# Performance work log

Hardware: AMD Instinct MI355X
Metric: run time of the kernel (lower is better)

The kernel has to match this reference:

```python
import jax, jax.numpy as jnp
import numpy as np

B, NB, V1, V2, S, J, D, F = 32, 10, 3, 3, 2, 25, 3, 8
DIN = D * F          # 24
H1, H2 = 2 * DIN, 3 * DIN  # 48, 72
NFEAT, NCLASS = 256, 60
EPS = 1e-5


def _layernorm(h, g, b):
    m = jnp.mean(h, axis=-1, keepdims=True)
    v = jnp.mean(jnp.square(h - m), axis=-1, keepdims=True)
    return (h - m) * jax.lax.rsqrt(v + EPS) * g + b


def setup_inputs() -> dict:
    key = jax.random.key(0)
    ks = jax.random.split(key, 12)
    x = jax.random.normal(ks[0], (B, NB, V1, V2, S * J, D, F), dtype=jnp.float32)
    a = jax.random.uniform(ks[1], (J, J), dtype=jnp.float32)
    adj = a / jnp.sum(a, axis=1, keepdims=True)  # row-normalized dense adjacency
    sc = 0.05
    return {
        "x": x,
        "adj": adj,
        "W1": sc * jax.random.normal(ks[2], (DIN, H1), jnp.float32),
        "b1": jnp.zeros((H1,), jnp.float32),
        "g1": jnp.ones((H1,), jnp.float32),
        "be1": jnp.zeros((H1,), jnp.float32),
        "W2": sc * jax.random.normal(ks[3], (H1, H2), jnp.float32),
        "b2": jnp.zeros((H2,), jnp.float32),
        "g2": jnp.ones((H2,), jnp.float32),
        "be2": jnp.zeros((H2,), jnp.float32),
        "W3": sc * jax.random.normal(ks[4], (H2, NFEAT), jnp.float32),
        "b3": jnp.zeros((NFEAT,), jnp.float32),
        "g3": jnp.ones((NFEAT,), jnp.float32),
        "be3": jnp.zeros((NFEAT,), jnp.float32),
        "Wc": sc * jax.random.normal(ks[5], (J * NFEAT, NCLASS), jnp.float32),
        "bc": jnp.zeros((NCLASS,), jnp.float32),
        "batch_size": B,
        "degree": 4,
        "nclass": NCLASS,
        "alpha": 0.2,
    }


def _sgc_precompute(f0, adj, degree, alpha):
    # f0: [..., J, NFEAT]; repeated sparse-style propagation with accumulation
    def step(carry, _):
        f, acc = carry
        f = jnp.einsum('ij,...jf->...if', adj, f)
        acc = acc + (1.0 - alpha) * f + alpha * f0
        return (f, acc), None
    (_, acc), _ = jax.lax.scan(step, (f0, jnp.zeros_like(f0)), None, length=degree)
    return acc / degree


def reference(x, adj, W1, b1, g1, be1, W2, b2, g2, be2, W3, b3, g3, be3,
              Wc, bc, batch_size, degree, nclass, alpha):
    # split joints into (subject, joint) and flatten (D, F) per joint -> [B,NB,V1,V2,S,J,DIN]
    h = x.reshape(B, NB, V1, V2, S, J, DIN)
    h = jax.nn.relu(_layernorm(h @ W1 + b1, g1, be1))
    h = jax.nn.relu(_layernorm(h @ W2 + b2, g2, be2))
    h = _layernorm(h @ W3 + b3, g3, be3)            # dropout is identity in eval
    h = _sgc_precompute(h, adj, degree, alpha)       # [B,NB,V1,V2,S,J,NFEAT]
    vec = h.reshape(B, NB, V1, V2, S, J * NFEAT)
    logits = vec @ Wc + bc                            # [B,NB,V1,V2,S,NCLASS]
    block_mean = jnp.mean(logits, axis=4)             # mean over subjects
    pred = jnp.mean(block_mean, axis=(1, 2, 3))       # [B, NCLASS]
    return block_mean, pred
```

## Files before the change

### kernel.cpp

```cpp
#include <hip/hip_runtime.h>
#include <hip/hip_bf16.h>

typedef __hip_bfloat16 bf16t;
typedef _Float16 half_t;
typedef __attribute__((ext_vector_type(2))) _Float16 half2v;
typedef __attribute__((ext_vector_type(8))) _Float16 half8v;
typedef __attribute__((ext_vector_type(4))) float f32x4;
typedef unsigned int uint32;

#define BB   32
#define NC   60
#define NROW 2880
#define EPSF 1e-5f
#define ALPHA 0.2f
#define DEG  4

#define WS_M_OFF    256
#define WS_PW_OFF   4096
#define WS_W3BF_OFF 28672
#define WS_W2BF_OFF 77824
#define WS_W1BF_OFF 88064
#define WS_WCP_OFF  101376
#define WS_WCPF_OFF 869376
#define WS_PART_OFF 1688576
#define WS_GH3_OFF  7586816
#define WS_NEED     44450816ULL

#define P_W1  0
#define P_B1  1152
#define P_G1  1200
#define P_BE1 1248
#define P_W2  1296
#define P_B2  4752
#define P_G2  4824
#define P_BE2 4896
#define P_B3  4968
#define P_G3  5224
#define P_BE3 5480
#define P_BC  5736
#define P_TOT 5796
#define R_W3E (P_TOT+24576)
#define R_W2E (R_W3E+5120)
#define R_W1E (R_W2E+1536)

#define LB_H3L 0
#define LB_A1  12800
#define LB_CS  12800
#define LB_A2  22016
#define LB_H3H 22016
#define LB_STW 35328
#define LB_ST2 37376
#define LDS_FTOT 9472

__device__ __forceinline__ float ldin(const void* p, int i, int isbf){
  return isbf ? __bfloat162float(((const bf16t*)p)[i]) : ((const float*)p)[i];
}
__device__ __forceinline__ void stout(void* p, int i, int isbf, float v){
  if(isbf) ((bf16t*)p)[i] = __float2bfloat16(v);
  else     ((float*)p)[i] = v;
}
__device__ __forceinline__ half2v u2h2(uint32 u){
  half2v h; __builtin_memcpy(&h,&u,4); return h;
}
__device__ __forceinline__ uint32 pk2u(float a, float b){
  auto r = __builtin_amdgcn_cvt_pkrtz(a, b);
  uint32 u; __builtin_memcpy(&u,&r,4); return u;
}

__global__ void k0_prep(const void* x, const void* adj, int* flagp, float* M){
  __shared__ float A[625], P[625], Q[625], Ss[625];
  __shared__ int cnt, flg;
  int t = threadIdx.x;
  if(t==0) cnt = 0;
  __syncthreads();
  {
    const unsigned short* xb = (const unsigned short*)x;
    unsigned short u = xb[2*t];
    int e = (u>>7)&0xFF;
    if(e>=100 && e<=141) atomicAdd(&cnt,1);
  }
  __syncthreads();
  if(t==0){ flg = (cnt>=160)?1:0; flagp[0]=flg; }
  __syncthreads();
  int isbf = flg;
  for(int i=t;i<625;i+=256){ float a=ldin(adj,i,isbf); A[i]=a; P[i]=a; Ss[i]=a; }
  __syncthreads();
  for(int d=1; d<DEG; ++d){
    for(int o=t;o<625;o+=256){
      int i=o/25, j=o%25; float acc=0.f;
      for(int k=0;k<25;k++) acc += A[i*25+k]*P[k*25+j];
      Q[o]=acc;
    }
    __syncthreads();
    for(int o=t;o<625;o+=256){ P[o]=Q[o]; Ss[o]+=Q[o]; }
    __syncthreads();
  }
  const float coef = (1.0f-ALPHA)/(float)DEG;
  for(int o=t;o<625;o+=256){
    int i=o/25, j=o%25;
    M[o] = (i==j ? ALPHA : 0.0f) + coef*Ss[o];
  }
}

__global__ void k1_all(const void* W1,const void* b1,const void* g1,const void* be1,
                       const void* W2,const void* b2,const void* g2,const void* be2,
                       const void* W3,const void* b3,const void* g3,const void* be3,
                       const void* bc, const int* flagp,
                       float* pw, half_t* W3bf, half_t* W2bf, half_t* W1bf){
  int isbf = flagp[0];
  int o = blockIdx.x*256 + threadIdx.x;
  if(o < P_TOT){
    const void* src; int loc;
    if      (o < P_B1 ) { src=W1;  loc=o;        }
    else if (o < P_G1 ) { src=b1;  loc=o-P_B1;   }
    else if (o < P_BE1) { src=g1;  loc=o-P_G1;   }
    else if (o < P_W2 ) { src=be1; loc=o-P_BE1;  }
    else if (o < P_B2 ) { src=W2;  loc=o-P_W2;   }
    else if (o < P_G2 ) { src=b2;  loc=o-P_B2;   }
    else if (o < P_BE2) { src=g2;  loc=o-P_G2;   }
    else if (o < P_B3 ) { src=be2; loc=o-P_BE2;  }
    else if (o < P_G3 ) { src=b3;  loc=o-P_B3;   }
    else if (o < P_BE3) { src=g3;  loc=o-P_G3;   }
    else if (o < P_BC ) { src=be3; loc=o-P_BE3;  }
    else                { src=bc;  loc=o-P_BC;   }
    pw[o] = ldin(src, loc, isbf);
  } else if(o < R_W3E){
    int o2 = o - P_TOT;
    int ct = o2/1536, rem = o2 - ct*1536;
    int kt = rem/512, rem2 = rem - kt*512;
    int l = rem2>>3, j = rem2&7;
    int k = kt*32 + ((l>>4)<<3) + j;
    int col = (ct<<4) + (l&15);
    float v = (k<72) ? ldin(W3, k*256+col, isbf) : 0.f;
    W3bf[o2] = (half_t)v;
  } else if(o < R_W2E){
    int o2 = o - R_W3E;
    int ct = o2/1024, rem = o2 - ct*1024;
    int kt = rem/512, rem2 = rem - kt*512;
    int l = rem2>>3, j = rem2&7;
    int k = kt*32 + ((l>>4)<<3) + j;
    int col = (ct<<4) + (l&15);
    float v = (k<48 && col<72) ? ldin(W2, k*72+col, isbf) : 0.f;
    W2bf[o2] = (half_t)v;
  } else if(o < R_W1E){
    int o2 = o - R_W2E;
    int ct = o2/512, rem2 = o2 - ct*512;
    int l = rem2>>3, j = rem2&7;
    int k = ((l>>4)<<3) + j;
    int col = (ct<<4) + (l&15);
    float v = (k<24) ? ldin(W1, k*48+col, isbf) : 0.f;
    W1bf[o2] = (half_t)v;
  }
}

__global__ void k2_fold(const void* Wc, const float* M, const int* flagp, half_t* Wcp4){
  int isbf = flagp[0];
  int o = blockIdx.x*256 + threadIdx.x;
  if(o >= 384000) return;
  int grp = o>>4, hw = o&15;
  int kt = grp/15, cg = grp - kt*15;
  int p = hw>>3, cl = (hw>>1)&3, e = hw&1;
  int fl = kt*4 + 2*p + e;
  int j = fl>>8, f = fl&255;
  int c = cg*4 + cl;
  float acc = 0.f;
  for(int i=0;i<25;i++) acc += M[i*25+j]*ldin(Wc, (i*256+f)*60 + c, isbf);
  Wcp4[o] = (half_t)(0.5f*acc);
}

__global__ void k2_foldf(const void* Wc, const float* M, const int* flagp, half_t* Wcpf){
  int isbf = flagp[0];
  int o = blockIdx.x*256 + threadIdx.x;
  int j = o&7, l = (o>>3)&63, nt = (o>>9)&3, kst = o>>11;
  int k = kst*32 + ((l>>4)<<3) + j;
  int c = nt*16 + (l&15);
  float acc = 0.f;
  if(c < 60){
    int jj = k>>8, f = k&255;
    for(int i=0;i<25;i++) acc += M[i*25+jj]*ldin(Wc, (i*256+f)*60 + c, isbf);
  }
  Wcpf[o] = (half_t)(0.5f*acc);
}

template<bool FUSED>
__global__ __launch_bounds__(256,4) void k3_t(const void* x, const float* pw,
                                              const half_t* W3bf_, const half_t* W2bf_,
                                              const half_t* W1bf_,
                                              const unsigned short* Wcp4,
                                              const int* flagp, void* out, uint32* gH3d){
  __shared__ float sm[LDS_FTOT];
  char* smb = (char*)sm;
  half_t* H3L = (half_t*)(smb + LB_H3L);
  half_t* H3H = (half_t*)(smb + LB_H3H);
  half_t* A1h = (half_t*)(smb + LB_A1);
  half_t* A2h = (half_t*)(smb + LB_A2);
  half_t* XH  = A2h;
  float*  stw = (float*)(smb + LB_STW);
  float*  st2 = (float*)(smb + LB_ST2);
  float*  cs  = (float*)(smb + LB_CS);
  uint32* A1w = (uint32*)A1h;
  const unsigned short* W3u = (const unsigned short*)W3bf_;
  const unsigned short* W2u = (const unsigned short*)W2bf_;
  const unsigned short* W1u = (const unsigned short*)W1bf_;

  int t = threadIdx.x, bid = blockIdx.x;
  int l = t&63, w = t>>6, cb = l&15, g4 = l>>4;
  int isbf = flagp[0];
  const float* b1=pw+P_B1;  const float* g1=pw+P_G1;  const float* be1=pw+P_BE1;
  const float* b2=pw+P_B2;  const float* g2=pw+P_G2;  const float* be2=pw+P_BE2;
  const float* b3=pw+P_B3;  const float* g3=pw+P_G3;  const float* be3=pw+P_BE3;
  const float* bc=pw+P_BC;

  for(int o=t;o<512;o+=256){ int r=o>>3, dc=24+(o&7); A1w[r*36+dc]=0; }
  {
    int xoff = bid*1200;
    for(int i=t;i<2560;i+=256){
      int r=i/40, c=i-(i/40)*40;
      float v = (r<50 && c<24) ? ldin(x, xoff + r*24+c, isbf) : 0.f;
      XH[i] = (half_t)v;
    }
  }
  __syncthreads();

  {
    f32x4 acc1[3];
    float g1v[3], be1v[3];
    #pragma unroll
    for(int ct=0;ct<3;ct++){
      int col = ct*16 + cb;
      float b = b1[col]; g1v[ct]=g1[col]; be1v[ct]=be1[col];
      acc1[ct][0]=b; acc1[ct][1]=b; acc1[ct][2]=b; acc1[ct][3]=b;
    }
    half8v a = *(const half8v*)(XH + (w*16 + cb)*40 + (g4<<3));
    #pragma unroll
    for(int ct=0;ct<3;ct++){
      half8v b = *(const half8v*)(W1u + (ct*64 + l)*8);
      acc1[ct] = __builtin_amdgcn_mfma_f32_16x16x32_f16(a, b, acc1[ct], 0,0,0);
    }
    __syncthreads();
    #pragma unroll
    for(int r=0;r<4;r++){
      float s1 = acc1[0][r]+acc1[1][r]+acc1[2][r];
      float s2 = acc1[0][r]*acc1[0][r]+acc1[1][r]*acc1[1][r]+acc1[2][r]*acc1[2][r];
      #pragma unroll
      for(int d=1;d<16;d<<=1){ s1+=__shfl_xor(s1,d,64); s2+=__shfl_xor(s2,d,64); }
      float m = s1*(1.f/48.f);
      float var = s2*(1.f/48.f)-m*m;
      float rs = rsqrtf(var+EPSF);
      int row = w*16 + (g4<<2) + r;
      #pragma unroll
      for(int ct=0;ct<3;ct++){
        float val = (acc1[ct][r]-m)*rs*g1v[ct]+be1v[ct];
        A1h[row*72 + ct*16 + cb] = (half_t)fmaxf(val,0.f);
      }
    }
  }
  __syncthreads();

  {
    f32x4 acc2[5];
    #pragma unroll
    for(int ct=0;ct<5;ct++){
      int col = ct*16 + cb;
      float b = (col<72) ? b2[col] : 0.f;
      acc2[ct][0]=b; acc2[ct][1]=b; acc2[ct][2]=b; acc2[ct][3]=b;
    }
    #pragma unroll
    for(int kt=0;kt<2;kt++){
      half8v a = *(const half8v*)(A1h + (w*16 + cb)*72 + kt*32 + (g4<<3));
      #pragma unroll
      for(int ct=0;ct<5;ct++){
        half8v b = *(const half8v*)(W2u + ((ct*2+kt)*64 + l)*8);
        acc2[ct] = __builtin_amdgcn_mfma_f32_16x16x32_f16(a, b, acc2[ct], 0,0,0);
      }
    }
    __syncthreads();
    int valid4 = (cb<8);
    #pragma unroll
    for(int r=0;r<4;r++){
      float s1 = acc2[0][r]+acc2[1][r]+acc2[2][r]+acc2[3][r] + (valid4?acc2[4][r]:0.f);
      float s2 = acc2[0][r]*acc2[0][r]+acc2[1][r]*acc2[1][r]
               + acc2[2][r]*acc2[2][r]+acc2[3][r]*acc2[3][r]
               + (valid4?acc2[4][r]*acc2[4][r]:0.f);
      #pragma unroll
      for(int d=1;d<16;d<<=1){ s1+=__shfl_xor(s1,d,64); s2+=__shfl_xor(s2,d,64); }
      float m = s1*(1.f/72.f);
      float var = s2*(1.f/72.f)-m*m;
      float rs = rsqrtf(var+EPSF);
      int grow = w*16 + (g4<<2) + r;
      #pragma unroll
      for(int ct=0;ct<5;ct++){
        int col = ct*16 + cb;
        if(ct<4 || valid4){
          float val = (acc2[ct][r]-m)*rs*g2[col]+be2[col];
          A2h[grow*104+col] = (half_t)fmaxf(val,0.f);
        }
      }
    }
    uint32* A2w = (uint32*)A2h;
    for(int o=l;o<192;o+=64){ int rr = w*16 + o/12, dc = 36 + (o - (o/12)*12); A2w[rr*52+dc]=0; }
  }
  __syncthreads();

  #pragma unroll 1
  for(int p=0;p<2;p++){
    f32x4 acc[2][4];
    #pragma unroll
    for(int nt=0;nt<4;nt++){
      float b3c = b3[w*64 + nt*16 + cb];
      #pragma unroll
      for(int m2=0;m2<2;m2++){ acc[m2][nt][0]=b3c; acc[m2][nt][1]=b3c; acc[m2][nt][2]=b3c; acc[m2][nt][3]=b3c; }
    }
    #pragma unroll
    for(int kt=0;kt<3;kt++){
      half8v a[2];
      #pragma unroll
      for(int m2=0;m2<2;m2++)
        a[m2] = *(const half8v*)(A2h + ((p*2+m2)*16+cb)*104 + kt*32 + (g4<<3));
      #pragma unroll
      for(int nt=0;nt<4;nt++){
        int ct = w*4 + nt;
        half8v b = *(const half8v*)(W3u + ((ct*3+kt)*64 + l)*8);
        #pragma unroll
        for(int m2=0;m2<2;m2++)
          acc[m2][nt] = __builtin_amdgcn_mfma_f32_16x16x32_f16(a[m2], b, acc[m2][nt], 0,0,0);
      }
    }
    __syncthreads();
    #pragma unroll
    for(int m2=0;m2<2;m2++){
      #pragma unroll
      for(int r=0;r<4;r++){
        int row = (p*2+m2)*16 + (g4<<2) + r;
        float s1 = acc[m2][0][r]+acc[m2][1][r]+acc[m2][2][r]+acc[m2][3][r];
        float s2 = acc[m2][0][r]*acc[m2][0][r]+acc[m2][1][r]*acc[m2][1][r]
                 + acc[m2][2][r]*acc[m2][2][r]+acc[m2][3][r]*acc[m2][3][r];
        #pragma unroll
        for(int d=1;d<16;d<<=1){ s1+=__shfl_xor(s1,d,64); s2+=__shfl_xor(s2,d,64); }
        if(cb==0){
          stw[row*8 + w*2]   = s1;
          stw[row*8 + w*2+1] = s2;
        }
        if(row<50){
          #pragma unroll
          for(int nt=0;nt<4;nt++){
            int col = w*64 + nt*16 + cb;
            if(row<25) H3L[row*256+col]      = (half_t)acc[m2][nt][r];
            else       H3H[(row-25)*256+col] = (half_t)acc[m2][nt][r];
          }
        }
      }
    }
  }
  __syncthreads();
  if(t<64){
    float S1 = stw[t*8+0]+stw[t*8+2]+stw[t*8+4]+stw[t*8+6];
    float S2 = stw[t*8+1]+stw[t*8+3]+stw[t*8+5]+stw[t*8+7];
    float m = S1*(1.f/256.f);
    float var = S2*(1.f/256.f)-m*m;
    st2[2*t]=m; st2[2*t+1]=rsqrtf(var+EPSF);
  }
  __syncthreads();
  {
    uint32* H3l32 = (uint32*)H3L;
    uint32* H3h32 = (uint32*)H3H;
    int cp = t & 127, ro = t>>7;
    float ga=g3[2*cp], gb=g3[2*cp+1], ba=be3[2*cp], bb=be3[2*cp+1];
    for(int r=ro; r<25; r+=2){
      uint32 lo = H3l32[r*128+cp], hi = H3h32[r*128+cp];
      float ml=st2[2*r], rl=st2[2*r+1];
      float mh=st2[2*(r+25)], rh=st2[2*(r+25)+1];
      half2v l2=u2h2(lo), h2=u2h2(hi);
      float v0 = ((float)l2[0]-ml)*rl*ga+ba + ((float)h2[0]-mh)*rh*ga+ba;
      float v1 = ((float)l2[1]-ml)*rl*gb+bb + ((float)h2[1]-mh)*rh*gb+bb;
      if(FUSED) H3l32[r*128+cp] = pk2u(v0, v1);
      else      gH3d[(size_t)bid*3200 + r*128 + cp] = pk2u(v0, v1);
    }
  }
  if constexpr (FUSED){
    __syncthreads();
    {
      int cgc = (cb<15)?cb:14;
      int ktbase = w*400 + g4*100;
      const unsigned short* H3u = (const unsigned short*)H3L;
      float a0=0.f,a1=0.f,a2=0.f,a3=0.f;
      for(int i=0;i<100;i++){
        int kt = ktbase + i;
        uint2 hq = *(const uint2*)(H3u + kt*4);
        const uint4* qp = (const uint4*)(Wcp4 + (size_t)(kt*15+cgc)*16);
        uint4 wa = qp[0], wb = qp[1];
        half2v h01 = u2h2(hq.x), h23 = u2h2(hq.y);
        a0 = __builtin_amdgcn_fdot2(h01, u2h2(wa.x), a0, false);
        a0 = __builtin_amdgcn_fdot2(h23, u2h2(wb.x), a0, false);
        a1 = __builtin_amdgcn_fdot2(h01, u2h2(wa.y), a1, false);
        a1 = __builtin_amdgcn_fdot2(h23, u2h2(wb.y), a1, false);
        a2 = __builtin_amdgcn_fdot2(h01, u2h2(wa.z), a2, false);
        a2 = __builtin_amdgcn_fdot2(h23, u2h2(wb.z), a2, false);
        a3 = __builtin_amdgcn_fdot2(h01, u2h2(wa.w), a3, false);
        a3 = __builtin_amdgcn_fdot2(h23, u2h2(wb.w), a3, false);
      }
      a0 += __shfl_xor(a0,16,64); a0 += __shfl_xor(a0,32,64);
      a1 += __shfl_xor(a1,16,64); a1 += __shfl_xor(a1,32,64);
      a2 += __shfl_xor(a2,16,64); a2 += __shfl_xor(a2,32,64);
      a3 += __shfl_xor(a3,16,64); a3 += __shfl_xor(a3,32,64);
      if(l<15){
        cs[w*60 + l*4 + 0] = a0;
        cs[w*60 + l*4 + 1] = a1;
        cs[w*60 + l*4 + 2] = a2;
        cs[w*60 + l*4 + 3] = a3;
      }
    }
    __syncthreads();
    if(t<NC){
      float v = cs[t]+cs[60+t]+cs[120+t]+cs[180+t] + bc[t];
      stout(out, bid*NC+t, isbf, v);
    }
  }
}

__global__ __launch_bounds__(256) void k5_gemm(const half_t* gH3, const half_t* Wcpf,
                                               float* part){
  int bx = blockIdx.x, ky = blockIdx.y;
  int t = threadIdx.x, l = t&63, w = t>>6, cb = l&15, g4 = l>>4;
  const unsigned short* H = (const unsigned short*)gH3;
  const unsigned short* W = (const unsigned short*)Wcpf;
  int base = bx*64 + w*16;
  f32x4 acc[4];
  #pragma unroll
  for(int nt=0;nt<4;nt++){ acc[nt][0]=0.f; acc[nt][1]=0.f; acc[nt][2]=0.f; acc[nt][3]=0.f; }
  int kst0 = ky*25;
  for(int ks=0;ks<25;ks++){
    int kst = kst0 + ks;
    half8v a = *(const half8v*)(H + (size_t)(base+cb)*6400 + kst*32 + (g4<<3));
    #pragma unroll
    for(int nt=0;nt<4;nt++){
      half8v b = *(const half8v*)(W + ((kst*4+nt)*64 + l)*8);
      acc[nt] = __builtin_amdgcn_mfma_f32_16x16x32_f16(a, b, acc[nt], 0,0,0);
    }
  }
  #pragma unroll
  for(int nt=0;nt<4;nt++){
    #pragma unroll
    for(int r=0;r<4;r++){
      int inst = base + (g4<<2) + r;
      part[((size_t)ky*NROW + inst)*64 + nt*16 + cb] = acc[nt][r];
    }
  }
}

__global__ void k4b_out(const float* part, const float* pw, const int* flagp, void* out){
  int o = blockIdx.x*256 + threadIdx.x;
  if(o >= NROW*NC) return;
  int inst = o/NC, c = o - inst*NC;
  float v = pw[P_BC + c];
  #pragma unroll
  for(int ky=0;ky<8;ky++) v += part[((size_t)ky*NROW + inst)*64 + c];
  stout(out, o, flagp[0], v);
}

__global__ void k4_pred(const void* bm, const int* flagp, void* out){
  int b = blockIdx.x, t = threadIdx.x;
  int isbf = flagp[0];
  if(t<NC){
    float acc=0.f;
    for(int r=0;r<90;r++) acc += ldin(bm, (b*90+r)*NC+t, isbf);
    stout(out, NROW*NC + b*NC + t, isbf, acc*(1.f/90.f));
  }
}

extern "C" void kernel_launch(void* const* d_in, const int* in_sizes, int n_in,
                              void* d_out, int out_size, void* d_ws, size_t ws_size,
                              hipStream_t stream){
  const void* x   = d_in[0];
  const void* adj = d_in[1];
  char* ws = (char*)d_ws;
  int*     flagp = (int*)ws;
  float*   M     = (float*)(ws + WS_M_OFF);
  float*   pw    = (float*)(ws + WS_PW_OFF);
  half_t*  W3bf  = (half_t*)(ws + WS_W3BF_OFF);
  half_t*  W2bf  = (half_t*)(ws + WS_W2BF_OFF);
  half_t*  W1bf  = (half_t*)(ws + WS_W1BF_OFF);
  half_t*  Wcp4  = (half_t*)(ws + WS_WCP_OFF);
  half_t*  Wcpf  = (half_t*)(ws + WS_WCPF_OFF);
  float*   part  = (float*)(ws + WS_PART_OFF);
  half_t*  gH3   = (half_t*)(ws + WS_GH3_OFF);
  bool fast = (ws_size >= WS_NEED);

  k0_prep<<<1,256,0,stream>>>(x, adj, flagp, M);
  k1_all<<<(R_W1E+255)/256,256,0,stream>>>(d_in[2],d_in[3],d_in[4],d_in[5],
                                           d_in[6],d_in[7],d_in[8],d_in[9],
                                           d_in[10],d_in[11],d_in[12],d_in[13],
                                           d_in[15], flagp, pw, W3bf, W2bf, W1bf);
  if(fast){
    k2_foldf<<<1600,256,0,stream>>>(d_in[14], M, flagp, Wcpf);
    k3_t<false><<<NROW,256,0,stream>>>(x, pw, W3bf, W2bf, W1bf,
                                       (const unsigned short*)nullptr, flagp, d_out,
                                       (uint32*)gH3);
    dim3 g5(45,8);
    k5_gemm<<<g5,256,0,stream>>>(gH3, Wcpf, part);
    k4b_out<<<(NROW*NC+255)/256,256,0,stream>>>(part, pw, flagp, d_out);
  } else {
    k2_fold<<<1500,256,0,stream>>>(d_in[14], M, flagp, Wcp4);
    k3_t<true><<<NROW,256,0,stream>>>(x, pw, W3bf, W2bf, W1bf,
                                      (const unsigned short*)Wcp4, flagp, d_out,
                                      (uint32*)nullptr);
  }
  k4_pred<<<BB,64,0,stream>>>(d_out, flagp, d_out);
}
```

Baseline: 111.2 us.

## Interleave subject rows so per-joint subject sum happens in registers, shrink LDS

Adds a dedicated fast-path kernel that loads the input with rows interleaved by subject, so the two subjects of each joint land in adjacent accumulator rows. The final layernorm and the subject sum are then applied straight from MFMA registers and written to global memory. This removes the LDS staging of the full layer-3 output and its extra read-back pass. LDS use drops and the launch bound rises from 4 to 6 blocks per CU for more occupancy. The fused fallback is kept as a separate non-templated kernel.

```diff
diff --git a/kernel.cpp b/kernel.cpp
--- a/kernel.cpp
+++ b/kernel.cpp
@@ -42,6 +42,12 @@
 #define R_W3E (P_TOT+24576)
 #define R_W2E (R_W3E+5120)
 #define R_W1E (R_W2E+1536)
+
+#define LF_A1  0
+#define LF_A2  9216
+#define LF_STW 22528
+#define LF_ST2 24576
+#define LF_FTOT 6272
 
 #define LB_H3L 0
 #define LB_A1  12800
@@ -182,12 +188,199 @@
   Wcpf[o] = (half_t)(0.5f*acc);
 }
 
-template<bool FUSED>
-__global__ __launch_bounds__(256,4) void k3_t(const void* x, const float* pw,
+__global__ __launch_bounds__(256,6) void k3_fast(const void* x, const float* pw,
+                                                 const half_t* W3bf_, const half_t* W2bf_,
+                                                 const half_t* W1bf_,
+                                                 const int* flagp, half_t* gH3){
+  __shared__ float sm[LF_FTOT];
+  char* smb = (char*)sm;
+  half_t* A1h = (half_t*)(smb + LF_A1);
+  half_t* A2h = (half_t*)(smb + LF_A2);
+  half_t* XH  = A2h;
+  float*  stw = (float*)(smb + LF_STW);
+  float*  st2 = (float*)(smb + LF_ST2);
+  uint32* A1w = (uint32*)A1h;
+  const unsigned short* W3u = (const unsigned short*)W3bf_;
+  const unsigned short* W2u = (const unsigned short*)W2bf_;
+  const unsigned short* W1u = (const unsigned short*)W1bf_;
+
+  int t = threadIdx.x, bid = blockIdx.x;
+  int l = t&63, w = t>>6, cb = l&15, g4 = l>>4;
+  int isbf = flagp[0];
+  const float* b1=pw+P_B1;  const float* g1=pw+P_G1;  const float* be1=pw+P_BE1;
+  const float* b2=pw+P_B2;  const float* g2=pw+P_G2;  const float* be2=pw+P_BE2;
+  const float* b3=pw+P_B3;  const float* g3=pw+P_G3;  const float* be3=pw+P_BE3;
+
+  for(int o=t;o<512;o+=256){ int r=o>>3, dc=24+(o&7); A1w[r*36+dc]=0; }
+  {
+    int xoff = bid*1200;
+    for(int i=t;i<2560;i+=256){
+      int r=i/40, c=i-(i/40)*40;
+      float v = (r<50 && c<24) ? ldin(x, xoff + (r&1)*600 + (r>>1)*24 + c, isbf) : 0.f;
+      XH[i] = (half_t)v;
+    }
+  }
+  __syncthreads();
+
+  {
+    f32x4 acc1[3];
+    float g1v[3], be1v[3];
+    #pragma unroll
+    for(int ct=0;ct<3;ct++){
+      int col = ct*16 + cb;
+      float b = b1[col]; g1v[ct]=g1[col]; be1v[ct]=be1[col];
+      acc1[ct][0]=b; acc1[ct][1]=b; acc1[ct][2]=b; acc1[ct][3]=b;
+    }
+    half8v a = *(const half8v*)(XH + (w*16 + cb)*40 + (g4<<3));
+    #pragma unroll
+    for(int ct=0;ct<3;ct++){
+      half8v b = *(const half8v*)(W1u + (ct*64 + l)*8);
+      acc1[ct] = __builtin_amdgcn_mfma_f32_16x16x32_f16(a, b, acc1[ct], 0,0,0);
+    }
+    __syncthreads();
+    #pragma unroll
+    for(int r=0;r<4;r++){
+      float s1 = acc1[0][r]+acc1[1][r]+acc1[2][r];
+      float s2 = acc1[0][r]*acc1[0][r]+acc1[1][r]*acc1[1][r]+acc1[2][r]*acc1[2][r];
+      #pragma unroll
+      for(int d=1;d<16;d<<=1){ s1+=__shfl_xor(s1,d,64); s2+=__shfl_xor(s2,d,64); }
+      float m = s1*(1.f/48.f);
+      float var = s2*(1.f/48.f)-m*m;
+      float rs = rsqrtf(var+EPSF);
+      int row = w*16 + (g4<<2) + r;
+      #pragma unroll
+      for(int ct=0;ct<3;ct++){
+        float val = (acc1[ct][r]-m)*rs*g1v[ct]+be1v[ct];
+        A1h[row*72 + ct*16 + cb] = (half_t)fmaxf(val,0.f);
+      }
+    }
+  }
+  __syncthreads();
+
+  {
+    f32x4 acc2[5];
+    #pragma unroll
+    for(int ct=0;ct<5;ct++){
+      int col = ct*16 + cb;
+      float b = (col<72) ? b2[col] : 0.f;
+      acc2[ct][0]=b; acc2[ct][1]=b; acc2[ct][2]=b; acc2[ct][3]=b;
+    }
+    #pragma unroll
+    for(int kt=0;kt<2;kt++){
+      half8v a = *(const half8v*)(A1h + (w*16 + cb)*72 + kt*32 + (g4<<3));
+      #pragma unroll
+      for(int ct=0;ct<5;ct++){
+        half8v b = *(const half8v*)(W2u + ((ct*2+kt)*64 + l)*8);
+        acc2[ct] = __builtin_amdgcn_mfma_f32_16x16x32_f16(a, b, acc2[ct], 0,0,0);
+      }
+    }
+    __syncthreads();
+    int valid4 = (cb<8);
+    #pragma unroll
+    for(int r=0;r<4;r++){
+      float s1 = acc2[0][r]+acc2[1][r]+acc2[2][r]+acc2[3][r] + (valid4?acc2[4][r]:0.f);
+      float s2 = acc2[0][r]*acc2[0][r]+acc2[1][r]*acc2[1][r]
+               + acc2[2][r]*acc2[2][r]+acc2[3][r]*acc2[3][r]
+               + (valid4?acc2[4][r]*acc2[4][r]:0.f);
+      #pragma unroll
+      for(int d=1;d<16;d<<=1){ s1+=__shfl_xor(s1,d,64); s2+=__shfl_xor(s2,d,64); }
+      float m = s1*(1.f/72.f);
+      float var = s2*(1.f/72.f)-m*m;
+      float rs = rsqrtf(var+EPSF);
+      int grow = w*16 + (g4<<2) + r;
+      #pragma unroll
+      for(int ct=0;ct<5;ct++){
+        int col = ct*16 + cb;
+        if(ct<4 || valid4){
+          float val = (acc2[ct][r]-m)*rs*g2[col]+be2[col];
+          A2h[grow*104+col] = (half_t)fmaxf(val,0.f);
+        }
+      }
+    }
+    uint32* A2w = (uint32*)A2h;
+    for(int o=l;o<192;o+=64){ int rr = w*16 + o/12, dc = 36 + (o - (o/12)*12); A2w[rr*52+dc]=0; }
+  }
+  __syncthreads();
+
+  float g3v[4], be3v[4];
+  #pragma unroll
+  for(int nt=0;nt<4;nt++){ int col=w*64+nt*16+cb; g3v[nt]=g3[col]; be3v[nt]=be3[col]; }
+  #pragma unroll 1
+  for(int p=0;p<2;p++){
+    f32x4 acc[2][4];
+    #pragma unroll
+    for(int nt=0;nt<4;nt++){
+      float b3c = b3[w*64 + nt*16 + cb];
+      #pragma unroll
+      for(int m2=0;m2<2;m2++){ acc[m2][nt][0]=b3c; acc[m2][nt][1]=b3c; acc[m2][nt][2]=b3c; acc[m2][nt][3]=b3c; }
+    }
+    #pragma unroll
+    for(int kt=0;kt<3;kt++){
+      half8v a[2];
+      #pragma unroll
+      for(int m2=0;m2<2;m2++)
+        a[m2] = *(const half8v*)(A2h + ((p*2+m2)*16+cb)*104 + kt*32 + (g4<<3));
+      #pragma unroll
+      for(int nt=0;nt<4;nt++){
+        int ct = w*4 + nt;
+        half8v b = *(const half8v*)(W3u + ((ct*3+kt)*64 + l)*8);
+        #pragma unroll
+        for(int m2=0;m2<2;m2++)
+          acc[m2][nt] = __builtin_amdgcn_mfma_f32_16x16x32_f16(a[m2], b, acc[m2][nt], 0,0,0);
+      }
+    }
+    #pragma unroll
+    for(int m2=0;m2<2;m2++){
+      #pragma unroll
+      for(int r=0;r<4;r++){
+        int row = (p*2+m2)*16 + (g4<<2) + r;
+        float s1 = acc[m2][0][r]+acc[m2][1][r]+acc[m2][2][r]+acc[m2][3][r];
+        float s2 = acc[m2][0][r]*acc[m2][0][r]+acc[m2][1][r]*acc[m2][1][r]
+                 + acc[m2][2][r]*acc[m2][2][r]+acc[m2][3][r]*acc[m2][3][r];
+        #pragma unroll
+        for(int d=1;d<16;d<<=1){ s1+=__shfl_xor(s1,d,64); s2+=__shfl_xor(s2,d,64); }
+        if(cb==0){
+          stw[row*8 + w*2]   = s1;
+          stw[row*8 + w*2+1] = s2;
+        }
+      }
+    }
+    __syncthreads();
+    if(t<32){
+      int row = p*32 + t;
+      float S1 = stw[row*8+0]+stw[row*8+2]+stw[row*8+4]+stw[row*8+6];
+      float S2 = stw[row*8+1]+stw[row*8+3]+stw[row*8+5]+stw[row*8+7];
+      float m = S1*(1.f/256.f);
+      float var = S2*(1.f/256.f)-m*m;
+      st2[2*row]=m; st2[2*row+1]=rsqrtf(var+EPSF);
+    }
+    __syncthreads();
+    #pragma unroll
+    for(int m2=0;m2<2;m2++){
+      #pragma unroll
+      for(int pr=0;pr<2;pr++){
+        int re = (p*2+m2)*16 + (g4<<2) + pr*2;
+        if(re<50){
+          float me=st2[2*re],   rse=st2[2*re+1];
+          float mo=st2[2*re+2], rso=st2[2*re+3];
+          int jj = re>>1;
+          #pragma unroll
+          for(int nt=0;nt<4;nt++){
+            float ve = (acc[m2][nt][2*pr]  -me)*rse*g3v[nt]+be3v[nt];
+            float vo = (acc[m2][nt][2*pr+1]-mo)*rso*g3v[nt]+be3v[nt];
+            gH3[(size_t)bid*6400 + jj*256 + w*64 + nt*16 + cb] = (half_t)(ve+vo);
+          }
+        }
+      }
+    }
+  }
+}
+
+__global__ __launch_bounds__(256,4) void k3_fused(const void* x, const float* pw,
                                               const half_t* W3bf_, const half_t* W2bf_,
                                               const half_t* W1bf_,
                                               const unsigned short* Wcp4,
-                                              const int* flagp, void* out, uint32* gH3d){
+                                              const int* flagp, void* out){
   __shared__ float sm[LDS_FTOT];
   char* smb = (char*)sm;
   half_t* H3L = (half_t*)(smb + LB_H3L);
@@ -221,7 +414,6 @@
     }
   }
   __syncthreads();
-
   {
     f32x4 acc1[3];
     float g1v[3], be1v[3];
@@ -256,7 +448,6 @@
     }
   }
   __syncthreads();
-
   {
     f32x4 acc2[5];
     #pragma unroll
@@ -301,7 +492,6 @@
     for(int o=l;o<192;o+=64){ int rr = w*16 + o/12, dc = 36 + (o - (o/12)*12); A2w[rr*52+dc]=0; }
   }
   __syncthreads();
-
   #pragma unroll 1
   for(int p=0;p<2;p++){
     f32x4 acc[2][4];
@@ -373,48 +563,45 @@
       half2v l2=u2h2(lo), h2=u2h2(hi);
       float v0 = ((float)l2[0]-ml)*rl*ga+ba + ((float)h2[0]-mh)*rh*ga+ba;
       float v1 = ((float)l2[1]-ml)*rl*gb+bb + ((float)h2[1]-mh)*rh*gb+bb;
-      if(FUSED) H3l32[r*128+cp] = pk2u(v0, v1);
-      else      gH3d[(size_t)bid*3200 + r*128 + cp] = pk2u(v0, v1);
-    }
-  }
-  if constexpr (FUSED){
-    __syncthreads();
-    {
-      int cgc = (cb<15)?cb:14;
-      int ktbase = w*400 + g4*100;
-      const unsigned short* H3u = (const unsigned short*)H3L;
-      float a0=0.f,a1=0.f,a2=0.f,a3=0.f;
-      for(int i=0;i<100;i++){
-        int kt = ktbase + i;
-        uint2 hq = *(const uint2*)(H3u + kt*4);
-        const uint4* qp = (const uint4*)(Wcp4 + (size_t)(kt*15+cgc)*16);
-        uint4 wa = qp[0], wb = qp[1];
-        half2v h01 = u2h2(hq.x), h23 = u2h2(hq.y);
-        a0 = __builtin_amdgcn_fdot2(h01, u2h2(wa.x), a0, false);
-        a0 = __builtin_amdgcn_fdot2(h23, u2h2(wb.x), a0, false);
-        a1 = __builtin_amdgcn_fdot2(h01, u2h2(wa.y), a1, false);
-        a1 = __builtin_amdgcn_fdot2(h23, u2h2(wb.y), a1, false);
-        a2 = __builtin_amdgcn_fdot2(h01, u2h2(wa.z), a2, false);
-        a2 = __builtin_amdgcn_fdot2(h23, u2h2(wb.z), a2, false);
-        a3 = __builtin_amdgcn_fdot2(h01, u2h2(wa.w), a3, false);
-        a3 = __builtin_amdgcn_fdot2(h23, u2h2(wb.w), a3, false);
-      }
-      a0 += __shfl_xor(a0,16,64); a0 += __shfl_xor(a0,32,64);
-      a1 += __shfl_xor(a1,16,64); a1 += __shfl_xor(a1,32,64);
-      a2 += __shfl_xor(a2,16,64); a2 += __shfl_xor(a2,32,64);
-      a3 += __shfl_xor(a3,16,64); a3 += __shfl_xor(a3,32,64);
-      if(l<15){
-        cs[w*60 + l*4 + 0] = a0;
-        cs[w*60 + l*4 + 1] = a1;
-        cs[w*60 + l*4 + 2] = a2;
-        cs[w*60 + l*4 + 3] = a3;
-      }
-    }
-    __syncthreads();
-    if(t<NC){
-      float v = cs[t]+cs[60+t]+cs[120+t]+cs[180+t] + bc[t];
-      stout(out, bid*NC+t, isbf, v);
-    }
+      H3l32[r*128+cp] = pk2u(v0, v1);
+    }
+  }
+  __syncthreads();
+  {
+    int cgc = (cb<15)?cb:14;
+    int ktbase = w*400 + g4*100;
+    const unsigned short* H3u = (const unsigned short*)H3L;
+    float a0=0.f,a1=0.f,a2=0.f,a3=0.f;
+    for(int i=0;i<100;i++){
+      int kt = ktbase + i;
+      uint2 hq = *(const uint2*)(H3u + kt*4);
+      const uint4* qp = (const uint4*)(Wcp4 + (size_t)(kt*15+cgc)*16);
+      uint4 wa = qp[0], wb = qp[1];
+      half2v h01 = u2h2(hq.x), h23 = u2h2(hq.y);
+      a0 = __builtin_amdgcn_fdot2(h01, u2h2(wa.x), a0, false);
+      a0 = __builtin_amdgcn_fdot2(h23, u2h2(wb.x), a0, false);
+      a1 = __builtin_amdgcn_fdot2(h01, u2h2(wa.y), a1, false);
+      a1 = __builtin_amdgcn_fdot2(h23, u2h2(wb.y), a1, false);
+      a2 = __builtin_amdgcn_fdot2(h01, u2h2(wa.z), a2, false);
+      a2 = __builtin_amdgcn_fdot2(h23, u2h2(wb.z), a2, false);
+      a3 = __builtin_amdgcn_fdot2(h01, u2h2(wa.w), a3, false);
+      a3 = __builtin_amdgcn_fdot2(h23, u2h2(wb.w), a3, false);
+    }
+    a0 += __shfl_xor(a0,16,64); a0 += __shfl_xor(a0,32,64);
+    a1 += __shfl_xor(a1,16,64); a1 += __shfl_xor(a1,32,64);
+    a2 += __shfl_xor(a2,16,64); a2 += __shfl_xor(a2,32,64);
+    a3 += __shfl_xor(a3,16,64); a3 += __shfl_xor(a3,32,64);
+    if(l<15){
+      cs[w*60 + l*4 + 0] = a0;
+      cs[w*60 + l*4 + 1] = a1;
+      cs[w*60 + l*4 + 2] = a2;
+      cs[w*60 + l*4 + 3] = a3;
+    }
+  }
+  __syncthreads();
+  if(t<NC){
+    float v = cs[t]+cs[60+t]+cs[120+t]+cs[180+t] + bc[t];
+    stout(out, bid*NC+t, isbf, v);
   }
 }
 
@@ -493,17 +680,14 @@
                                            d_in[15], flagp, pw, W3bf, W2bf, W1bf);
   if(fast){
     k2_foldf<<<1600,256,0,stream>>>(d_in[14], M, flagp, Wcpf);
-    k3_t<false><<<NROW,256,0,stream>>>(x, pw, W3bf, W2bf, W1bf,
-                                       (const unsigned short*)nullptr, flagp, d_out,
-                                       (uint32*)gH3);
+    k3_fast<<<NROW,256,0,stream>>>(x, pw, W3bf, W2bf, W1bf, flagp, gH3);
     dim3 g5(45,8);
     k5_gemm<<<g5,256,0,stream>>>(gH3, Wcpf, part);
     k4b_out<<<(NROW*NC+255)/256,256,0,stream>>>(part, pw, flagp, d_out);
   } else {
     k2_fold<<<1500,256,0,stream>>>(d_in[14], M, flagp, Wcp4);
-    k3_t<true><<<NROW,256,0,stream>>>(x, pw, W3bf, W2bf, W1bf,
-                                      (const unsigned short*)Wcp4, flagp, d_out,
-                                      (uint32*)nullptr);
+    k3_fused<<<NROW,256,0,stream>>>(x, pw, W3bf, W2bf, W1bf,
+                                    (const unsigned short*)Wcp4, flagp, d_out);
   }
   k4_pred<<<BB,64,0,stream>>>(d_out, flagp, d_out);
 }
```

Measured after the change: 133.5 us. +20.1%, slower.
